# Performance work log

Hardware: AMD Instinct MI355X
Metric: run time of the kernel (lower is better)

The kernel has to match this reference:

```python
import jax, jax.numpy as jnp
import numpy as np
from jax import lax

H = 64          # GRU hidden size
OUT_STEPS = 20  # output_seq_size


def _maxpool2(x):
    # x: [N, C, H, W] -> 2x2 max pool, stride 2, VALID
    return lax.reduce_window(x, -jnp.inf, lax.max, (1, 1, 2, 2), (1, 1, 2, 2), 'VALID')


def _conv(x, w, b):
    # NCHW / OIHW, VALID, stride 1
    y = lax.conv_general_dilated(x, w, (1, 1), 'VALID',
                                 dimension_numbers=('NCHW', 'OIHW', 'NCHW'))
    return y + b[None, :, None, None]


def _gru_step(h, x, wih, whh, bih, bhh):
    # PyTorch GRU gate order: r, z, n
    gi = x @ wih.T + bih            # [B, 3H]
    gh = h @ whh.T + bhh            # [B, 3H]
    i_r, i_z, i_n = jnp.split(gi, 3, axis=-1)
    h_r, h_z, h_n = jnp.split(gh, 3, axis=-1)
    r = jax.nn.sigmoid(i_r + h_r)
    z = jax.nn.sigmoid(i_z + h_z)
    n = jnp.tanh(i_n + r * h_n)
    return (1.0 - z) * n + z * h


def setup_inputs() -> dict:
    key = jax.random.key(0)
    ks = jax.random.split(key, 20)
    B, T = 1024, 31
    s = 0.1
    return {
        'bbox_seq': jax.random.normal(ks[0], (B, T, 4), jnp.float32),
        'head_seq': jax.random.uniform(ks[1], (B, T, 32, 32), jnp.float32),
        'conv1_w': jax.random.normal(ks[2], (4, 1, 3, 3), jnp.float32) * s,
        'conv1_b': jax.random.normal(ks[3], (4,), jnp.float32) * s,
        'conv2_w': jax.random.normal(ks[4], (10, 4, 3, 3), jnp.float32) * s,
        'conv2_b': jax.random.normal(ks[5], (10,), jnp.float32) * s,
        'fc_w': jax.random.normal(ks[6], (5, 360), jnp.float32) * s,
        'fc_b': jax.random.normal(ks[7], (5,), jnp.float32) * s,
        'enc_wih': jax.random.normal(ks[8], (3 * H, 9), jnp.float32) * s,
        'enc_whh': jax.random.normal(ks[9], (3 * H, H), jnp.float32) * s,
        'enc_bih': jax.random.normal(ks[10], (3 * H,), jnp.float32) * s,
        'enc_bhh': jax.random.normal(ks[11], (3 * H,), jnp.float32) * s,
        'dec_wih': jax.random.normal(ks[12], (3 * H, 4), jnp.float32) * s,
        'dec_whh': jax.random.normal(ks[13], (3 * H, H), jnp.float32) * s,
        'dec_bih': jax.random.normal(ks[14], (3 * H,), jnp.float32) * s,
        'dec_bhh': jax.random.normal(ks[15], (3 * H,), jnp.float32) * s,
        'lin_w': jax.random.normal(ks[16], (4, H), jnp.float32) * s,
        'lin_b': jax.random.normal(ks[17], (4,), jnp.float32) * s,
    }


def reference(bbox_seq, head_seq, conv1_w, conv1_b, conv2_w, conv2_b, fc_w, fc_b,
              enc_wih, enc_whh, enc_bih, enc_bhh,
              dec_wih, dec_whh, dec_bih, dec_bhh, lin_w, lin_b):
    B, T = bbox_seq.shape[0], bbox_seq.shape[1]
    L = T - 1  # encoder sequence length

    # offset: last bbox, broadcast over OUT_STEPS -> [B, OUT_STEPS, 4]
    offset = jnp.broadcast_to(bbox_seq[:, -1][:, None, :], (B, OUT_STEPS, 4))

    diffs = bbox_seq[:, 1:] - bbox_seq[:, :-1]  # [B, L, 4] (dropout p=0 -> identity)

    # --- ConvEncoder on all head crops at once ---
    imgs = head_seq[:, :-1].reshape(B * L, 1, 32, 32)
    x = jax.nn.relu(_conv(imgs, conv1_w, conv1_b))   # [BL, 4, 30, 30]
    x = _maxpool2(x)                                  # [BL, 4, 15, 15]
    x = jax.nn.relu(_conv(x, conv2_w, conv2_b))       # [BL, 10, 13, 13]
    x = _maxpool2(x)                                  # [BL, 10, 6, 6]
    emb = x.reshape(B * L, -1) @ fc_w.T + fc_b        # [BL, 5]
    emb = emb.reshape(B, L, -1)

    enc_in = jnp.concatenate([diffs, emb], axis=2)    # [B, L, 9]

    # --- GRU encoder (scan over time) ---
    def enc_step(h, x_t):
        h = _gru_step(h, x_t, enc_wih, enc_whh, enc_bih, enc_bhh)
        return h, None
    h0 = jnp.zeros((B, H), enc_in.dtype)
    hn, _ = lax.scan(enc_step, h0, jnp.swapaxes(enc_in, 0, 1))

    def dec_step(carry, _):
        h, prev_x = carry
        h = _gru_step(h, prev_x, dec_wih, dec_whh, dec_bih, dec_bhh)
        x_new = h @ lin_w.T + lin_b + prev_x
        return (h, x_new), x_new
    (_, _), outs = lax.scan(dec_step, (hn, diffs[:, -1]), None, length=OUT_STEPS)
    out = jnp.swapaxes(outs, 0, 1)                    # [B, OUT_STEPS, 4]

    return jnp.cumsum(out, axis=1) + offset
```

## Files before the change

kernel.cpp:

```cpp
#include <hip/hip_runtime.h>
#include <hip/hip_bf16.h>


#define B_    1024
#define L_    30
#define H_    64

__device__ __forceinline__ float sigmoid_f(float v) {
    return 1.f / (1.f + __expf(-v));
}
__device__ __forceinline__ float tanh_f(float v) {
    v = fminf(fmaxf(v, -15.f), 15.f);
    float e = __expf(2.f * v);
    return (e - 1.f) / (e + 1.f);
}
__device__ __forceinline__ void load4_lds(float* r, const float* p) {
    float2 a = *(const float2*)p;
    float2 b = *(const float2*)(p + 2);
    r[0] = a.x; r[1] = a.y; r[2] = b.x; r[3] = b.y;
}

__global__ __launch_bounds__(64) void conv_embed_kernel(
    const float* __restrict__ bbox,
    const float* __restrict__ head,
    const float* __restrict__ c1w, const float* __restrict__ c1b,
    const float* __restrict__ c2w, const float* __restrict__ c2b,
    const float* __restrict__ fcw, const float* __restrict__ fcb,
    float* __restrict__ enc_in)
{
    const int img = blockIdx.x;
    const int b = img / L_;
    const int l = img % L_;
    const int tid = threadIdx.x;

    __shared__ float s_img[32 * 32];
    __shared__ float s_p1[4 * 15 * 16];
    __shared__ float s_p2[360];
    __shared__ float s_red[60];

    {
        const float4* src = (const float4*)(head + ((size_t)b * 31 + (size_t)l) * 1024);
        float4* dst = (float4*)s_img;
        #pragma unroll
        for (int i = 0; i < 4; ++i) dst[tid + 64 * i] = src[tid + 64 * i];
    }
    __syncthreads();

    if (tid < 60) {
        const int c = tid / 15, px = tid % 15;
        const int x0 = 2 * px;
        float w[9];
        #pragma unroll
        for (int k = 0; k < 9; ++k) w[k] = c1w[c * 9 + k];
        const float bias = c1b[c];

        float r0[4], r1[4], r2[4], r3[4];
        load4_lds(r0, s_img + 0 * 32 + x0);
        load4_lds(r1, s_img + 1 * 32 + x0);
        #pragma unroll
        for (int py = 0; py < 15; ++py) {
            load4_lds(r2, s_img + (2 * py + 2) * 32 + x0);
            load4_lds(r3, s_img + (2 * py + 3) * 32 + x0);
            float a00 = bias, a01 = bias, a10 = bias, a11 = bias;
            #pragma unroll
            for (int kx = 0; kx < 3; ++kx) {
                const float w0 = w[kx], w1 = w[3 + kx], w2 = w[6 + kx];
                a00 = fmaf(w0, r0[kx],     fmaf(w1, r1[kx],     fmaf(w2, r2[kx],     a00)));
                a01 = fmaf(w0, r0[kx + 1], fmaf(w1, r1[kx + 1], fmaf(w2, r2[kx + 1], a01)));
                a10 = fmaf(w0, r1[kx],     fmaf(w1, r2[kx],     fmaf(w2, r3[kx],     a10)));
                a11 = fmaf(w0, r1[kx + 1], fmaf(w1, r2[kx + 1], fmaf(w2, r3[kx + 1], a11)));
            }
            a00 = fmaxf(a00, 0.f); a01 = fmaxf(a01, 0.f);
            a10 = fmaxf(a10, 0.f); a11 = fmaxf(a11, 0.f);
            s_p1[c * 240 + py * 16 + px] = fmaxf(fmaxf(a00, a01), fmaxf(a10, a11));
            #pragma unroll
            for (int q = 0; q < 4; ++q) { r0[q] = r2[q]; r1[q] = r3[q]; }
        }
    }
    __syncthreads();

    if (tid < 60) {
        const int c = tid / 6, px = tid % 6;
        const int x0 = 2 * px;
        float w[4][9];
        #pragma unroll
        for (int ic = 0; ic < 4; ++ic)
            #pragma unroll
            for (int k = 0; k < 9; ++k) w[ic][k] = c2w[(c * 4 + ic) * 9 + k];
        const float bias = c2b[c];

        float win[4][4][4];
        #pragma unroll
        for (int ic = 0; ic < 4; ++ic) {
            load4_lds(win[0][ic], s_p1 + ic * 240 + 0 * 16 + x0);
            load4_lds(win[1][ic], s_p1 + ic * 240 + 1 * 16 + x0);
        }
        #pragma unroll
        for (int py = 0; py < 6; ++py) {
            #pragma unroll
            for (int ic = 0; ic < 4; ++ic) {
                load4_lds(win[2][ic], s_p1 + ic * 240 + (2 * py + 2) * 16 + x0);
                load4_lds(win[3][ic], s_p1 + ic * 240 + (2 * py + 3) * 16 + x0);
            }
            float a00 = bias, a01 = bias, a10 = bias, a11 = bias;
            #pragma unroll
            for (int ic = 0; ic < 4; ++ic) {
                #pragma unroll
                for (int kx = 0; kx < 3; ++kx) {
                    const float w0 = w[ic][kx], w1 = w[ic][3 + kx], w2 = w[ic][6 + kx];
                    a00 = fmaf(w0, win[0][ic][kx],     fmaf(w1, win[1][ic][kx],     fmaf(w2, win[2][ic][kx],     a00)));
                    a01 = fmaf(w0, win[0][ic][kx + 1], fmaf(w1, win[1][ic][kx + 1], fmaf(w2, win[2][ic][kx + 1], a01)));
                    a10 = fmaf(w0, win[1][ic][kx],     fmaf(w1, win[2][ic][kx],     fmaf(w2, win[3][ic][kx],     a10)));
                    a11 = fmaf(w0, win[1][ic][kx + 1], fmaf(w1, win[2][ic][kx + 1], fmaf(w2, win[3][ic][kx + 1], a11)));
                }
            }
            a00 = fmaxf(a00, 0.f); a01 = fmaxf(a01, 0.f);
            a10 = fmaxf(a10, 0.f); a11 = fmaxf(a11, 0.f);
            s_p2[c * 36 + py * 6 + px] = fmaxf(fmaxf(a00, a01), fmaxf(a10, a11));
            #pragma unroll
            for (int ic = 0; ic < 4; ++ic)
                #pragma unroll
                for (int q = 0; q < 4; ++q) { win[0][ic][q] = win[2][ic][q]; win[1][ic][q] = win[3][ic][q]; }
        }
    }
    __syncthreads();

    if (tid < 60) {
        const int o = tid / 12, i0 = tid % 12;
        const float* wrow = fcw + o * 360;
        float acc = 0.f;
        #pragma unroll
        for (int k = 0; k < 30; ++k) {
            const int i = i0 + 12 * k;
            acc = fmaf(wrow[i], s_p2[i], acc);
        }
        s_red[tid] = acc;
    }
    __syncthreads();

    float* dst = enc_in + ((size_t)b * L_ + l) * 9;
    if (tid < 5) {
        float acc = fcb[tid];
        #pragma unroll
        for (int k = 0; k < 12; ++k) acc += s_red[tid * 12 + k];
        dst[4 + tid] = acc;
    } else if (tid >= 8 && tid < 12) {
        const int d = tid - 8;
        const float* bb = bbox + (size_t)b * 124 + (size_t)l * 4;
        dst[d] = bb[4 + d] - bb[d];
    }
}

__global__ __launch_bounds__(256) void gru_enc_kernel(
    const float* __restrict__ enc_in,
    const float* __restrict__ wih,
    const float* __restrict__ whh,
    const float* __restrict__ bih,
    const float* __restrict__ bhh,
    float* __restrict__ hn)
{
    const int b = blockIdx.x;
    const int tid = threadIdx.x;
    const int w = tid >> 6, j = tid & 63;

    float Wh[3][16];
    #pragma unroll
    for (int g = 0; g < 3; ++g) {
        const float* row = whh + (g * 64 + j) * 64 + w * 16;
        #pragma unroll
        for (int k = 0; k < 16; ++k) Wh[g][k] = row[k];
    }
    float Wi[3][9];
    #pragma unroll
    for (int g = 0; g < 3; ++g) {
        const float* row = wih + (g * 64 + j) * 9;
        #pragma unroll
        for (int k = 0; k < 9; ++k) Wi[g][k] = row[k];
    }
    const float bi0 = bih[j], bi1 = bih[64 + j], bi2 = bih[128 + j];
    const float bh0 = bhh[j], bh1 = bhh[64 + j], bh2 = bhh[128 + j];

    __shared__ float sp[2][4][3][64];
    float h = 0.f;
    const float* xp = enc_in + (size_t)b * (L_ * 9);

    for (int t = 0; t < L_; ++t) {
        const int pb = t & 1;
        float pr = 0.f, pz = 0.f, pn = 0.f;
        #pragma unroll
        for (int k = 0; k < 16; ++k) {
            const float hk = __shfl(h, w * 16 + k);
            pr = fmaf(Wh[0][k], hk, pr);
            pz = fmaf(Wh[1][k], hk, pz);
            pn = fmaf(Wh[2][k], hk, pn);
        }
        sp[pb][w][0][j] = pr;
        sp[pb][w][1][j] = pz;
        sp[pb][w][2][j] = pn;

        float x[9];
        #pragma unroll
        for (int k = 0; k < 9; ++k) x[k] = xp[t * 9 + k];
        float gr = bi0 + bh0, gz = bi1 + bh1, gni = bi2, gnh = bh2;
        #pragma unroll
        for (int k = 0; k < 9; ++k) {
            gr  = fmaf(Wi[0][k], x[k], gr);
            gz  = fmaf(Wi[1][k], x[k], gz);
            gni = fmaf(Wi[2][k], x[k], gni);
        }
        __syncthreads();
        #pragma unroll
        for (int ww = 0; ww < 4; ++ww) {
            gr  += sp[pb][ww][0][j];
            gz  += sp[pb][ww][1][j];
            gnh += sp[pb][ww][2][j];
        }
        const float r = sigmoid_f(gr);
        const float z = sigmoid_f(gz);
        const float n = tanh_f(gni + r * gnh);
        h = (1.f - z) * n + z * h;
    }
    if (w == 0) hn[(size_t)b * H_ + j] = h;
}

__global__ __launch_bounds__(256) void gru_dec_kernel(
    const float* __restrict__ bbox,
    const float* __restrict__ hn,
    const float* __restrict__ wih,
    const float* __restrict__ whh,
    const float* __restrict__ bih,
    const float* __restrict__ bhh,
    const float* __restrict__ linw,
    const float* __restrict__ linb,
    float* __restrict__ out)
{
    const int b = blockIdx.x;
    const int tid = threadIdx.x;
    const int w = tid >> 6, j = tid & 63;

    float Wh[3][16];
    #pragma unroll
    for (int g = 0; g < 3; ++g) {
        const float* row = whh + (g * 64 + j) * 64 + w * 16;
        #pragma unroll
        for (int k = 0; k < 16; ++k) Wh[g][k] = row[k];
    }
    float Wi[3][4];
    #pragma unroll
    for (int g = 0; g < 3; ++g) {
        const float* row = wih + (g * 64 + j) * 4;
        #pragma unroll
        for (int k = 0; k < 4; ++k) Wi[g][k] = row[k];
    }
    const float bi0 = bih[j], bi1 = bih[64 + j], bi2 = bih[128 + j];
    const float bh0 = bhh[j], bh1 = bhh[64 + j], bh2 = bhh[128 + j];
    const float lw0 = linw[j], lw1 = linw[64 + j], lw2 = linw[128 + j], lw3 = linw[192 + j];
    const float lb0 = linb[0], lb1 = linb[1], lb2 = linb[2], lb3 = linb[3];

    float h = hn[(size_t)b * H_ + j];
    const float* bb = bbox + (size_t)b * 124;
    float px0 = bb[120] - bb[116];
    float px1 = bb[121] - bb[117];
    float px2 = bb[122] - bb[118];
    float px3 = bb[123] - bb[119];
    const float of0 = bb[120], of1 = bb[121], of2 = bb[122], of3 = bb[123];
    float cs0 = 0.f, cs1 = 0.f, cs2 = 0.f, cs3 = 0.f;

    __shared__ float sp[2][4][3][64];
    float* outp = out + (size_t)b * 80;

    for (int t = 0; t < 20; ++t) {
        const int pb = t & 1;
        float pr = 0.f, pz = 0.f, pn = 0.f;
        #pragma unroll
        for (int k = 0; k < 16; ++k) {
            const float hk = __shfl(h, w * 16 + k);
            pr = fmaf(Wh[0][k], hk, pr);
            pz = fmaf(Wh[1][k], hk, pz);
            pn = fmaf(Wh[2][k], hk, pn);
        }
        sp[pb][w][0][j] = pr;
        sp[pb][w][1][j] = pz;
        sp[pb][w][2][j] = pn;

        float gr = bi0 + bh0, gz = bi1 + bh1, gni = bi2, gnh = bh2;
        gr  = fmaf(Wi[0][0], px0, fmaf(Wi[0][1], px1, fmaf(Wi[0][2], px2, fmaf(Wi[0][3], px3, gr))));
        gz  = fmaf(Wi[1][0], px0, fmaf(Wi[1][1], px1, fmaf(Wi[1][2], px2, fmaf(Wi[1][3], px3, gz))));
        gni = fmaf(Wi[2][0], px0, fmaf(Wi[2][1], px1, fmaf(Wi[2][2], px2, fmaf(Wi[2][3], px3, gni))));

        __syncthreads();
        #pragma unroll
        for (int ww = 0; ww < 4; ++ww) {
            gr  += sp[pb][ww][0][j];
            gz  += sp[pb][ww][1][j];
            gnh += sp[pb][ww][2][j];
        }
        const float r = sigmoid_f(gr);
        const float z = sigmoid_f(gz);
        const float n = tanh_f(gni + r * gnh);
        h = (1.f - z) * n + z * h;

        float v0 = lw0 * h, v1 = lw1 * h, v2 = lw2 * h, v3 = lw3 * h;
        #pragma unroll
        for (int s = 32; s > 0; s >>= 1) {
            v0 += __shfl_xor(v0, s);
            v1 += __shfl_xor(v1, s);
            v2 += __shfl_xor(v2, s);
            v3 += __shfl_xor(v3, s);
        }
        px0 = v0 + lb0 + px0;
        px1 = v1 + lb1 + px1;
        px2 = v2 + lb2 + px2;
        px3 = v3 + lb3 + px3;
        cs0 += px0; cs1 += px1; cs2 += px2; cs3 += px3;
        if (tid == 0) {
            outp[t * 4 + 0] = cs0 + of0;
            outp[t * 4 + 1] = cs1 + of1;
            outp[t * 4 + 2] = cs2 + of2;
            outp[t * 4 + 3] = cs3 + of3;
        }
    }
}

extern "C" void kernel_launch(void* const* d_in, const int* in_sizes, int n_in,
                              void* d_out, int out_size, void* d_ws, size_t ws_size,
                              hipStream_t stream) {
    (void)in_sizes; (void)n_in; (void)out_size; (void)ws_size;
    const float* bbox = (const float*)d_in[0];
    const float* head = (const float*)d_in[1];
    const float* c1w  = (const float*)d_in[2];
    const float* c1b  = (const float*)d_in[3];
    const float* c2w  = (const float*)d_in[4];
    const float* c2b  = (const float*)d_in[5];
    const float* fcw  = (const float*)d_in[6];
    const float* fcb  = (const float*)d_in[7];
    const float* ewih = (const float*)d_in[8];
    const float* ewhh = (const float*)d_in[9];
    const float* ebih = (const float*)d_in[10];
    const float* ebhh = (const float*)d_in[11];
    const float* dwih = (const float*)d_in[12];
    const float* dwhh = (const float*)d_in[13];
    const float* dbih = (const float*)d_in[14];
    const float* dbhh = (const float*)d_in[15];
    const float* linw = (const float*)d_in[16];
    const float* linb = (const float*)d_in[17];
    float* out = (float*)d_out;

    float* enc_in = (float*)d_ws;
    float* hn     = enc_in + (size_t)B_ * L_ * 9;

    conv_embed_kernel<<<B_ * L_, 64, 0, stream>>>(bbox, head, c1w, c1b, c2w, c2b,
                                                  fcw, fcb, enc_in);
    gru_enc_kernel<<<B_, 256, 0, stream>>>(enc_in, ewih, ewhh, ebih, ebhh, hn);
    gru_dec_kernel<<<B_, 256, 0, stream>>>(bbox, hn, dwih, dwhh, dbih, dbhh,
                                           linw, linb, out);
}
```

Before: 341.4 us.

## Repartition conv work across all threads and run GRU batches one per wavefront

The conv stages are rewritten so all 64 threads work: each thread computes one pooled pixel for all four conv1 channels, and conv2 is split into pixel and output-channel-pair units. Activations move to a channel-interleaved, padded shared layout, and conv2 weights are staged in shared memory. The GRU encoder and decoder now give each 64-lane wavefront one full batch row holding all 64 recurrent weights per gate in registers, which removes the cross-wave shared-memory reduction and per-step barrier. The costs are much higher register pressure (192 weight floats per thread) and a 64-step serial shuffle chain per timestep.

```diff
diff --git a/kernel.cpp b/kernel.cpp
--- a/kernel.cpp
+++ b/kernel.cpp
@@ -33,94 +33,129 @@
     const int l = img % L_;
     const int tid = threadIdx.x;
 
-    __shared__ float s_img[32 * 32];
-    __shared__ float s_p1[4 * 15 * 16];
+    __shared__ float s_img[32 * 36];
+    __shared__ float s_p1[15 * 17 * 4];
+    __shared__ float s_w2[10 * 4 * 12];
+    __shared__ float s_b2[10];
     __shared__ float s_p2[360];
-    __shared__ float s_red[60];
+    __shared__ float s_red[64];
 
     {
         const float4* src = (const float4*)(head + ((size_t)b * 31 + (size_t)l) * 1024);
-        float4* dst = (float4*)s_img;
-        #pragma unroll
-        for (int i = 0; i < 4; ++i) dst[tid + 64 * i] = src[tid + 64 * i];
+        #pragma unroll
+        for (int i = 0; i < 4; ++i) {
+            const int g = 4 * (tid + 64 * i);
+            float4 v = src[tid + 64 * i];
+            *(float4*)&s_img[(g >> 5) * 36 + (g & 31)] = v;
+        }
+        for (int idx = tid; idx < 360; idx += 64) {
+            const int oc = idx / 36, r = idx % 36;
+            const int ic = r / 9, k = r % 9;
+            s_w2[(oc * 4 + ic) * 12 + k] = c2w[idx];
+        }
+        if (tid < 10) s_b2[tid] = c2b[tid];
     }
     __syncthreads();
 
-    if (tid < 60) {
-        const int c = tid / 15, px = tid % 15;
-        const int x0 = 2 * px;
-        float w[9];
-        #pragma unroll
-        for (int k = 0; k < 9; ++k) w[k] = c1w[c * 9 + k];
-        const float bias = c1b[c];
-
-        float r0[4], r1[4], r2[4], r3[4];
-        load4_lds(r0, s_img + 0 * 32 + x0);
-        load4_lds(r1, s_img + 1 * 32 + x0);
-        #pragma unroll
-        for (int py = 0; py < 15; ++py) {
-            load4_lds(r2, s_img + (2 * py + 2) * 32 + x0);
-            load4_lds(r3, s_img + (2 * py + 3) * 32 + x0);
-            float a00 = bias, a01 = bias, a10 = bias, a11 = bias;
+    {
+        float w1[36], b1[4];
+        #pragma unroll
+        for (int k = 0; k < 36; ++k) w1[k] = c1w[k];
+        #pragma unroll
+        for (int k = 0; k < 4; ++k) b1[k] = c1b[k];
+
+        #pragma unroll
+        for (int it = 0; it < 4; ++it) {
+            const int p = tid + 64 * it;
+            if (p < 225) {
+                const int py = p / 15, px = p % 15;
+                const int y0 = 2 * py, x0 = 2 * px;
+                float r[4][4];
+                #pragma unroll
+                for (int rr = 0; rr < 4; ++rr)
+                    load4_lds(r[rr], &s_img[(y0 + rr) * 36 + x0]);
+                float4 outv;
+                #pragma unroll
+                for (int oc = 0; oc < 4; ++oc) {
+                    float a00 = b1[oc], a01 = b1[oc], a10 = b1[oc], a11 = b1[oc];
+                    #pragma unroll
+                    for (int ky = 0; ky < 3; ++ky) {
+                        #pragma unroll
+                        for (int kx = 0; kx < 3; ++kx) {
+                            const float w = w1[oc * 9 + ky * 3 + kx];
+                            a00 = fmaf(w, r[ky][kx],         a00);
+                            a01 = fmaf(w, r[ky][kx + 1],     a01);
+                            a10 = fmaf(w, r[ky + 1][kx],     a10);
+                            a11 = fmaf(w, r[ky + 1][kx + 1], a11);
+                        }
+                    }
+                    a00 = fmaxf(a00, 0.f); a01 = fmaxf(a01, 0.f);
+                    a10 = fmaxf(a10, 0.f); a11 = fmaxf(a11, 0.f);
+                    ((float*)&outv)[oc] = fmaxf(fmaxf(a00, a01), fmaxf(a10, a11));
+                }
+                *(float4*)&s_p1[(py * 17 + px) * 4] = outv;
+            }
+        }
+    }
+    __syncthreads();
+
+    #pragma unroll
+    for (int it = 0; it < 3; ++it) {
+        const int u = tid + 64 * it;
+        if (u < 180) {
+            const int pix = u / 5, ocp = u % 5;
+            const int ppy = pix / 6, ppx = pix % 6;
+            const int y0 = 2 * ppy, x0 = 2 * ppx;
+            float4 P[4][4];
             #pragma unroll
-            for (int kx = 0; kx < 3; ++kx) {
-                const float w0 = w[kx], w1 = w[3 + kx], w2 = w[6 + kx];
-                a00 = fmaf(w0, r0[kx],     fmaf(w1, r1[kx],     fmaf(w2, r2[kx],     a00)));
-                a01 = fmaf(w0, r0[kx + 1], fmaf(w1, r1[kx + 1], fmaf(w2, r2[kx + 1], a01)));
-                a10 = fmaf(w0, r1[kx],     fmaf(w1, r2[kx],     fmaf(w2, r3[kx],     a10)));
-                a11 = fmaf(w0, r1[kx + 1], fmaf(w1, r2[kx + 1], fmaf(w2, r3[kx + 1], a11)));
+            for (int rr = 0; rr < 4; ++rr)
+                #pragma unroll
+                for (int cc = 0; cc < 4; ++cc)
+                    P[rr][cc] = *(const float4*)&s_p1[((y0 + rr) * 17 + (x0 + cc)) * 4];
+
+            const int oc0 = 2 * ocp;
+            float a[2][4];
+            #pragma unroll
+            for (int o = 0; o < 2; ++o) {
+                const float bias = s_b2[oc0 + o];
+                #pragma unroll
+                for (int q = 0; q < 4; ++q) a[o][q] = bias;
             }
-            a00 = fmaxf(a00, 0.f); a01 = fmaxf(a01, 0.f);
-            a10 = fmaxf(a10, 0.f); a11 = fmaxf(a11, 0.f);
-            s_p1[c * 240 + py * 16 + px] = fmaxf(fmaxf(a00, a01), fmaxf(a10, a11));
-            #pragma unroll
-            for (int q = 0; q < 4; ++q) { r0[q] = r2[q]; r1[q] = r3[q]; }
-        }
-    }
-    __syncthreads();
-
-    if (tid < 60) {
-        const int c = tid / 6, px = tid % 6;
-        const int x0 = 2 * px;
-        float w[4][9];
-        #pragma unroll
-        for (int ic = 0; ic < 4; ++ic)
-            #pragma unroll
-            for (int k = 0; k < 9; ++k) w[ic][k] = c2w[(c * 4 + ic) * 9 + k];
-        const float bias = c2b[c];
-
-        float win[4][4][4];
-        #pragma unroll
-        for (int ic = 0; ic < 4; ++ic) {
-            load4_lds(win[0][ic], s_p1 + ic * 240 + 0 * 16 + x0);
-            load4_lds(win[1][ic], s_p1 + ic * 240 + 1 * 16 + x0);
-        }
-        #pragma unroll
-        for (int py = 0; py < 6; ++py) {
             #pragma unroll
             for (int ic = 0; ic < 4; ++ic) {
-                load4_lds(win[2][ic], s_p1 + ic * 240 + (2 * py + 2) * 16 + x0);
-                load4_lds(win[3][ic], s_p1 + ic * 240 + (2 * py + 3) * 16 + x0);
-            }
-            float a00 = bias, a01 = bias, a10 = bias, a11 = bias;
-            #pragma unroll
-            for (int ic = 0; ic < 4; ++ic) {
-                #pragma unroll
-                for (int kx = 0; kx < 3; ++kx) {
-                    const float w0 = w[ic][kx], w1 = w[ic][3 + kx], w2 = w[ic][6 + kx];
-                    a00 = fmaf(w0, win[0][ic][kx],     fmaf(w1, win[1][ic][kx],     fmaf(w2, win[2][ic][kx],     a00)));
-                    a01 = fmaf(w0, win[0][ic][kx + 1], fmaf(w1, win[1][ic][kx + 1], fmaf(w2, win[2][ic][kx + 1], a01)));
-                    a10 = fmaf(w0, win[1][ic][kx],     fmaf(w1, win[2][ic][kx],     fmaf(w2, win[3][ic][kx],     a10)));
-                    a11 = fmaf(w0, win[1][ic][kx + 1], fmaf(w1, win[2][ic][kx + 1], fmaf(w2, win[3][ic][kx + 1], a11)));
+                float wk[2][12];
+                #pragma unroll
+                for (int o = 0; o < 2; ++o) {
+                    const float* wb = &s_w2[((oc0 + o) * 4 + ic) * 12];
+                    *(float4*)&wk[o][0] = *(const float4*)&wb[0];
+                    *(float4*)&wk[o][4] = *(const float4*)&wb[4];
+                    *(float4*)&wk[o][8] = *(const float4*)&wb[8];
+                }
+                #pragma unroll
+                for (int ky = 0; ky < 3; ++ky) {
+                    #pragma unroll
+                    for (int kx = 0; kx < 3; ++kx) {
+                        const float p00 = ((const float*)&P[ky][kx])[ic];
+                        const float p01 = ((const float*)&P[ky][kx + 1])[ic];
+                        const float p10 = ((const float*)&P[ky + 1][kx])[ic];
+                        const float p11 = ((const float*)&P[ky + 1][kx + 1])[ic];
+                        #pragma unroll
+                        for (int o = 0; o < 2; ++o) {
+                            const float w = wk[o][ky * 3 + kx];
+                            a[o][0] = fmaf(w, p00, a[o][0]);
+                            a[o][1] = fmaf(w, p01, a[o][1]);
+                            a[o][2] = fmaf(w, p10, a[o][2]);
+                            a[o][3] = fmaf(w, p11, a[o][3]);
+                        }
+                    }
                 }
             }
-            a00 = fmaxf(a00, 0.f); a01 = fmaxf(a01, 0.f);
-            a10 = fmaxf(a10, 0.f); a11 = fmaxf(a11, 0.f);
-            s_p2[c * 36 + py * 6 + px] = fmaxf(fmaxf(a00, a01), fmaxf(a10, a11));
             #pragma unroll
-            for (int ic = 0; ic < 4; ++ic)
-                #pragma unroll
-                for (int q = 0; q < 4; ++q) { win[0][ic][q] = win[2][ic][q]; win[1][ic][q] = win[3][ic][q]; }
+            for (int o = 0; o < 2; ++o) {
+                float m0 = fmaxf(fmaxf(a[o][0], 0.f), fmaxf(a[o][1], 0.f));
+                float m1 = fmaxf(fmaxf(a[o][2], 0.f), fmaxf(a[o][3], 0.f));
+                s_p2[(oc0 + o) * 36 + ppy * 6 + ppx] = fmaxf(m0, m1);
+            }
         }
     }
     __syncthreads();
@@ -151,7 +186,7 @@
     }
 }
 
-__global__ __launch_bounds__(256) void gru_enc_kernel(
+__global__ __launch_bounds__(128) void gru_enc_kernel(
     const float* __restrict__ enc_in,
     const float* __restrict__ wih,
     const float* __restrict__ whh,
@@ -159,16 +194,15 @@
     const float* __restrict__ bhh,
     float* __restrict__ hn)
 {
-    const int b = blockIdx.x;
-    const int tid = threadIdx.x;
-    const int w = tid >> 6, j = tid & 63;
-
-    float Wh[3][16];
+    const int w = threadIdx.x >> 6, j = threadIdx.x & 63;
+    const int b = blockIdx.x * 2 + w;
+
+    float Wh[3][64];
     #pragma unroll
     for (int g = 0; g < 3; ++g) {
-        const float* row = whh + (g * 64 + j) * 64 + w * 16;
-        #pragma unroll
-        for (int k = 0; k < 16; ++k) Wh[g][k] = row[k];
+        const float4* row = (const float4*)(whh + (size_t)(g * 64 + j) * 64);
+        #pragma unroll
+        for (int k4 = 0; k4 < 16; ++k4) *(float4*)&Wh[g][4 * k4] = row[k4];
     }
     float Wi[3][9];
     #pragma unroll
@@ -180,50 +214,34 @@
     const float bi0 = bih[j], bi1 = bih[64 + j], bi2 = bih[128 + j];
     const float bh0 = bhh[j], bh1 = bhh[64 + j], bh2 = bhh[128 + j];
 
-    __shared__ float sp[2][4][3][64];
     float h = 0.f;
     const float* xp = enc_in + (size_t)b * (L_ * 9);
 
     for (int t = 0; t < L_; ++t) {
-        const int pb = t & 1;
-        float pr = 0.f, pz = 0.f, pn = 0.f;
-        #pragma unroll
-        for (int k = 0; k < 16; ++k) {
-            const float hk = __shfl(h, w * 16 + k);
-            pr = fmaf(Wh[0][k], hk, pr);
-            pz = fmaf(Wh[1][k], hk, pz);
-            pn = fmaf(Wh[2][k], hk, pn);
-        }
-        sp[pb][w][0][j] = pr;
-        sp[pb][w][1][j] = pz;
-        sp[pb][w][2][j] = pn;
-
-        float x[9];
-        #pragma unroll
-        for (int k = 0; k < 9; ++k) x[k] = xp[t * 9 + k];
         float gr = bi0 + bh0, gz = bi1 + bh1, gni = bi2, gnh = bh2;
         #pragma unroll
         for (int k = 0; k < 9; ++k) {
-            gr  = fmaf(Wi[0][k], x[k], gr);
-            gz  = fmaf(Wi[1][k], x[k], gz);
-            gni = fmaf(Wi[2][k], x[k], gni);
-        }
-        __syncthreads();
-        #pragma unroll
-        for (int ww = 0; ww < 4; ++ww) {
-            gr  += sp[pb][ww][0][j];
-            gz  += sp[pb][ww][1][j];
-            gnh += sp[pb][ww][2][j];
+            const float xk = xp[t * 9 + k];
+            gr  = fmaf(Wi[0][k], xk, gr);
+            gz  = fmaf(Wi[1][k], xk, gz);
+            gni = fmaf(Wi[2][k], xk, gni);
+        }
+        #pragma unroll
+        for (int k = 0; k < 64; ++k) {
+            const float hk = __shfl(h, k);
+            gr  = fmaf(Wh[0][k], hk, gr);
+            gz  = fmaf(Wh[1][k], hk, gz);
+            gnh = fmaf(Wh[2][k], hk, gnh);
         }
         const float r = sigmoid_f(gr);
         const float z = sigmoid_f(gz);
         const float n = tanh_f(gni + r * gnh);
         h = (1.f - z) * n + z * h;
     }
-    if (w == 0) hn[(size_t)b * H_ + j] = h;
-}
-
-__global__ __launch_bounds__(256) void gru_dec_kernel(
+    hn[(size_t)b * H_ + j] = h;
+}
+
+__global__ __launch_bounds__(128) void gru_dec_kernel(
     const float* __restrict__ bbox,
     const float* __restrict__ hn,
     const float* __restrict__ wih,
@@ -234,16 +252,15 @@
     const float* __restrict__ linb,
     float* __restrict__ out)
 {
-    const int b = blockIdx.x;
-    const int tid = threadIdx.x;
-    const int w = tid >> 6, j = tid & 63;
-
-    float Wh[3][16];
+    const int w = threadIdx.x >> 6, j = threadIdx.x & 63;
+    const int b = blockIdx.x * 2 + w;
+
+    float Wh[3][64];
     #pragma unroll
     for (int g = 0; g < 3; ++g) {
-        const float* row = whh + (g * 64 + j) * 64 + w * 16;
-        #pragma unroll
-        for (int k = 0; k < 16; ++k) Wh[g][k] = row[k];
+        const float4* row = (const float4*)(whh + (size_t)(g * 64 + j) * 64);
+        #pragma unroll
+        for (int k4 = 0; k4 < 16; ++k4) *(float4*)&Wh[g][4 * k4] = row[k4];
     }
     float Wi[3][4];
     #pragma unroll
@@ -266,34 +283,19 @@
     const float of0 = bb[120], of1 = bb[121], of2 = bb[122], of3 = bb[123];
     float cs0 = 0.f, cs1 = 0.f, cs2 = 0.f, cs3 = 0.f;
 
-    __shared__ float sp[2][4][3][64];
-    float* outp = out + (size_t)b * 80;
+    float4* outp = (float4*)(out + (size_t)b * 80);
 
     for (int t = 0; t < 20; ++t) {
-        const int pb = t & 1;
-        float pr = 0.f, pz = 0.f, pn = 0.f;
-        #pragma unroll
-        for (int k = 0; k < 16; ++k) {
-            const float hk = __shfl(h, w * 16 + k);
-            pr = fmaf(Wh[0][k], hk, pr);
-            pz = fmaf(Wh[1][k], hk, pz);
-            pn = fmaf(Wh[2][k], hk, pn);
-        }
-        sp[pb][w][0][j] = pr;
-        sp[pb][w][1][j] = pz;
-        sp[pb][w][2][j] = pn;
-
         float gr = bi0 + bh0, gz = bi1 + bh1, gni = bi2, gnh = bh2;
         gr  = fmaf(Wi[0][0], px0, fmaf(Wi[0][1], px1, fmaf(Wi[0][2], px2, fmaf(Wi[0][3], px3, gr))));
         gz  = fmaf(Wi[1][0], px0, fmaf(Wi[1][1], px1, fmaf(Wi[1][2], px2, fmaf(Wi[1][3], px3, gz))));
         gni = fmaf(Wi[2][0], px0, fmaf(Wi[2][1], px1, fmaf(Wi[2][2], px2, fmaf(Wi[2][3], px3, gni))));
-
-        __syncthreads();
-        #pragma unroll
-        for (int ww = 0; ww < 4; ++ww) {
-            gr  += sp[pb][ww][0][j];
-            gz  += sp[pb][ww][1][j];
-            gnh += sp[pb][ww][2][j];
+        #pragma unroll
+        for (int k = 0; k < 64; ++k) {
+            const float hk = __shfl(h, k);
+            gr  = fmaf(Wh[0][k], hk, gr);
+            gz  = fmaf(Wh[1][k], hk, gz);
+            gnh = fmaf(Wh[2][k], hk, gnh);
         }
         const float r = sigmoid_f(gr);
         const float z = sigmoid_f(gz);
@@ -313,12 +315,7 @@
         px2 = v2 + lb2 + px2;
         px3 = v3 + lb3 + px3;
         cs0 += px0; cs1 += px1; cs2 += px2; cs3 += px3;
-        if (tid == 0) {
-            outp[t * 4 + 0] = cs0 + of0;
-            outp[t * 4 + 1] = cs1 + of1;
-            outp[t * 4 + 2] = cs2 + of2;
-            outp[t * 4 + 3] = cs3 + of3;
-        }
+        if (j == 0) outp[t] = make_float4(cs0 + of0, cs1 + of1, cs2 + of2, cs3 + of3);
     }
 }
 
@@ -351,7 +348,7 @@
 
     conv_embed_kernel<<<B_ * L_, 64, 0, stream>>>(bbox, head, c1w, c1b, c2w, c2b,
                                                   fcw, fcb, enc_in);
-    gru_enc_kernel<<<B_, 256, 0, stream>>>(enc_in, ewih, ewhh, ebih, ebhh, hn);
-    gru_dec_kernel<<<B_, 256, 0, stream>>>(bbox, hn, dwih, dwhh, dbih, dbhh,
-                                           linw, linb, out);
-}
+    gru_enc_kernel<<<B_ / 2, 128, 0, stream>>>(enc_in, ewih, ewhh, ebih, ebhh, hn);
+    gru_dec_kernel<<<B_ / 2, 128, 0, stream>>>(bbox, hn, dwih, dwhh, dbih, dbhh,
+                                               linw, linb, out);
+}
```

Measured after the change: 394.8 us. 15.7% more time.
